# Performance work log

Hardware: AMD Instinct MI355X
Metric: run time of the kernel (lower is better)

Reference implementation:

```python
import jax, jax.numpy as jnp
import numpy as np

DIM = 64; NH = 4; WS = (2, 7, 7); FRAMES = 8
# torch code uses head_dim = dim // num_heads for BOTH attentions' scale
SCALE = (DIM // NH) ** -0.5

def _rel_pos_index(ws):
    coords = np.stack(np.meshgrid(np.arange(ws[0]), np.arange(ws[1]), np.arange(ws[2]), indexing='ij'))
    cf = coords.reshape(3, -1)
    rc = (cf[:, :, None] - cf[:, None, :]).transpose(1, 2, 0)
    rc[:, :, 0] += ws[0] - 1; rc[:, :, 1] += ws[1] - 1; rc[:, :, 2] += ws[2] - 1
    rc[:, :, 0] *= (2 * ws[1] - 1) * (2 * ws[2] - 1)
    rc[:, :, 1] *= 2 * ws[2] - 1
    return jnp.asarray(rc.sum(-1))

REL_S = _rel_pos_index(WS)              # (98, 98)
REL_T = _rel_pos_index((FRAMES, 1, 1))  # (8, 8)

def _ln(x, g, b, eps=1e-5):
    m = x.mean(-1, keepdims=True)
    v = ((x - m) ** 2).mean(-1, keepdims=True)
    return (x - m) * jax.lax.rsqrt(v + eps) * g + b

def _conv3d(x, w, b):
    y = jax.lax.conv_general_dilated(x, w, (1, 1, 1), [(1, 1)] * 3,
                                     dimension_numbers=('NCDHW', 'OIDHW', 'NCDHW'))
    return y + b[None, :, None, None, None]

def setup_inputs():
    key = jax.random.key(0)
    ks = jax.random.split(key, 16)
    B, D, H, W, C = 2, 8, 112, 112, DIM
    C2 = C // 2
    n = lambda i, shape: jax.random.normal(ks[i], shape, jnp.float32) * 0.02
    return dict(
        x=jax.random.normal(ks[0], (B, D, H, W, C), jnp.float32),
        mask_matrix=jnp.zeros((1, 98, 98), jnp.float32),
        g1=jnp.ones((C,), jnp.float32), b1=jnp.zeros((C,), jnp.float32),
        rpb_s=n(1, ((2*WS[0]-1)*(2*WS[1]-1)*(2*WS[2]-1), NH)),
        qkv_w_s=n(2, (C, 3*C)), qkv_b_s=jnp.zeros((3*C,), jnp.float32),
        proj_w_s=n(3, (C, C)), proj_b_s=jnp.zeros((C,), jnp.float32),
        rpb_t=n(4, (2*FRAMES-1, NH)),
        qkv_w_t=n(5, (C, 3*C2)), qkv_b_t=jnp.zeros((3*C2,), jnp.float32),
        proj_w_t=n(6, (C2, C)), proj_b_t=jnp.zeros((C,), jnp.float32),
        g2=jnp.ones((C,), jnp.float32), b2=jnp.zeros((C,), jnp.float32),
        p1c1_w=n(7, (C2, C2, 3, 3, 3)), p1c1_b=jnp.zeros((C2,), jnp.float32),
        p1c2_w=n(8, (C2, C2, 3, 3, 3)), p1c2_b=jnp.zeros((C2,), jnp.float32),
        p2c1_w=n(9, (C2, C2, 3, 3, 3)), p2c1_b=jnp.zeros((C2,), jnp.float32),
        p2c2_w=n(10, (C2, C2, 3, 3, 3)), p2c2_b=jnp.zeros((C2,), jnp.float32),
    )

def reference(x, mask_matrix, g1, b1, rpb_s, qkv_w_s, qkv_b_s, proj_w_s, proj_b_s,
              rpb_t, qkv_w_t, qkv_b_t, proj_w_t, proj_b_t, g2, b2,
              p1c1_w, p1c1_b, p1c2_w, p1c2_b, p2c1_w, p2c1_b, p2c2_w, p2c2_b):
    B, D, H, W, C = x.shape
    C2 = C // 2
    wd, wh, ww = WS
    N = wd * wh * ww
    shortcut = x
    h = _ln(x, g1, b1)
    # ---- space attention over (2,7,7) windows (shift=0, H/W/D divisible -> no pad/roll/mask) ----
    xw = h.reshape(B, D // wd, wd, H // wh, wh, W // ww, ww, C)
    xw = xw.transpose(0, 1, 3, 5, 2, 4, 6, 7).reshape(-1, N, C)  # (nW, N, C)
    nw = xw.shape[0]
    qkv = (xw @ qkv_w_s + qkv_b_s).reshape(nw, N, 3, NH, C // NH).transpose(2, 0, 3, 1, 4)
    q, k, v = qkv[0] * SCALE, qkv[1], qkv[2]
    attn = jnp.einsum('whnd,whmd->whnm', q, k)
    bias = rpb_s[REL_S.reshape(-1)].reshape(N, N, NH).transpose(2, 0, 1)
    attn = jax.nn.softmax(attn + bias[None], axis=-1)
    out = jnp.einsum('whnm,whmd->whnd', attn, v).transpose(0, 2, 1, 3).reshape(nw, N, C)
    out = out @ proj_w_s + proj_b_s
    space = out.reshape(B, D // wd, H // wh, W // ww, wd, wh, ww, C)
    space = space.transpose(0, 1, 4, 2, 5, 3, 6, 7).reshape(B, D, H, W, C)
    # ---- time attention over frames (qkv projects to C/2) ----
    xt = h.transpose(0, 2, 3, 1, 4).reshape(B * H * W, D, C)
    qkv_t = (xt @ qkv_w_t + qkv_b_t).reshape(-1, D, 3, NH, C2 // NH).transpose(2, 0, 3, 1, 4)
    qt, kt, vt = qkv_t[0] * SCALE, qkv_t[1], qkv_t[2]
    at = jnp.einsum('bhnd,bhmd->bhnm', qt, kt)
    bias_t = rpb_t[REL_T.reshape(-1)].reshape(D, D, NH).transpose(2, 0, 1)
    at = jax.nn.softmax(at + bias_t[None], axis=-1)
    ot = jnp.einsum('bhnm,bhmd->bhnd', at, vt).transpose(0, 2, 1, 3).reshape(-1, D, C2)
    ot = ot @ proj_w_t + proj_b_t  # (B*H*W, D, C)
    time = ot.reshape(B, H, W, D, C).transpose(0, 3, 1, 2, 4)
    x = shortcut + time + space
    # ---- GRFFNet conv FFN ----
    h2 = _ln(x, g2, b2).transpose(0, 4, 1, 2, 3)  # (B,C,D,H,W)
    x1, x2 = h2[:, :C2], h2[:, C2:]
    y1 = x1 + _conv3d(jax.nn.leaky_relu(_conv3d(x1, p1c1_w, p1c1_b)), p1c2_w, p1c2_b)
    x2 = x2 + y1
    y2 = x2 + _conv3d(jax.nn.leaky_relu(_conv3d(x2, p2c1_w, p2c1_b)), p2c2_w, p2c2_b)
    y = jnp.concatenate([y1, y2], axis=1).transpose(0, 2, 3, 4, 1)
    return x + y
```

## Files before the change

kernel.cpp:

```cpp
#include <hip/hip_runtime.h>
#include <hip/hip_bf16.h>

typedef unsigned short u16;
typedef unsigned int u32;
typedef __attribute__((ext_vector_type(8))) short s16x8;
typedef __attribute__((ext_vector_type(4))) float f32x4;

__device__ __forceinline__ u16 f2b(float v) {
  u32 bits = __float_as_uint(v);
  bits += 0x7fffu + ((bits >> 16) & 1u);
  return (u16)(bits >> 16);
}
__device__ __forceinline__ float b2f(u16 u) { return __uint_as_float(((u32)u) << 16); }
__device__ __forceinline__ float bflo(u32 w) { return __uint_as_float(w << 16); }
__device__ __forceinline__ float bfhi(u32 w) { return __uint_as_float(w & 0xffff0000u); }

__global__ __launch_bounds__(256) void k_ln(const float* __restrict__ x, const float* __restrict__ g,
    const float* __restrict__ b, float* __restrict__ hout, u16* __restrict__ xb) {
  int token = blockIdx.x * 4 + (threadIdx.x >> 6);
  int lane = threadIdx.x & 63;
  long base = (long)token * 64 + lane;
  float v = x[base];
  float s = v;
#pragma unroll
  for (int o = 32; o; o >>= 1) s += __shfl_xor(s, o);
  float m = s * 0.015625f;
  float d = v - m;
  float q = d * d;
#pragma unroll
  for (int o = 32; o; o >>= 1) q += __shfl_xor(q, o);
  float r = rsqrtf(q * 0.015625f + 1e-5f);
  float hv = d * r * g[lane] + b[lane];
  hout[base] = hv;
  if (lane < 32) xb[(long)token * 32 + lane] = f2b(hv);
}

__global__ __launch_bounds__(256) void k_prep(const float* __restrict__ pw, u16* __restrict__ pwb,
    const float* __restrict__ tqw, u16* __restrict__ twb,
    const float* __restrict__ sqw, u16* __restrict__ swb,
    const float* __restrict__ rpb, float* __restrict__ Bt) {
  int i = blockIdx.x * 256 + threadIdx.x;
  if (i < 4096) {
    int r = i & 7, q = i >> 3;
    int col = q & 15; q >>= 4;
    int lk = q & 1; q >>= 1;
    int nt = q & 3, hd = q >> 2;
    pwb[i] = f2b(pw[(hd * 16 + lk * 8 + r) * 64 + nt * 16 + col]);
  } else if (i < 10240) {
    int j = i - 4096;
    int kk = j & 31, q = j >> 5;
    int lm = q & 15, ksnt = q >> 4;
    int ks = ksnt & 1, nt = ksnt >> 1;
    twb[j] = f2b(tqw[(ks * 32 + kk) * 96 + nt * 16 + lm]);
  } else if (i < 22528) {
    int j = i - 10240;
    int kk = j & 31, q = j >> 5;
    int lm = q & 15, ksnt = q >> 4;
    int ks = ksnt & 1, nt = ksnt >> 1;
    swb[j] = f2b(sqw[(ks * 32 + kk) * 192 + nt * 16 + lm]);
  } else {
    int j = i - 22528;
    int m = j % 112, q = j / 112;
    int n = q % 112, hd = q / 112;
    float v = -1e30f;
    if (n < 98 && m < 98) {
      int dzn = n / 49, rn = n % 49, hyn = rn / 7, wxn = rn % 7;
      int dzm = m / 49, rm = m % 49, hym = rm / 7, wxm = rm % 7;
      int idx = (dzn - dzm + 1) * 169 + (hyn - hym + 6) * 13 + (wxn - wxm + 6);
      v = rpb[idx * 4 + hd];
    }
    Bt[j] = v;
  }
}

__global__ __launch_bounds__(256) void k_wprep(const float* __restrict__ w0, const float* __restrict__ w1,
    const float* __restrict__ w2, const float* __restrict__ w3, u16* __restrict__ WB) {
  int j = blockIdx.x * 256 + threadIdx.x;
  int c = j / 27648, j2 = j - c * 27648;
  const float* src = c == 0 ? w0 : c == 1 ? w1 : c == 2 ? w2 : w3;
  int co = j2 / 864, rem = j2 - co * 864, ci = rem / 27, kk = rem - ci * 27;
  WB[c * 27648 + kk * 1024 + co * 32 + ci] = f2b(src[j2]);
}

__global__ __launch_bounds__(256) void k_fused1(const float* __restrict__ x,
    const float* __restrict__ g1, const float* __restrict__ b1,
    const u16* __restrict__ swb, const float* __restrict__ sqb,
    const u16* __restrict__ twb, const float* __restrict__ tqb,
    float* __restrict__ acc, u16* __restrict__ Qg, u16* __restrict__ Kg,
    u16* __restrict__ Vg, u16* __restrict__ T) {
  int l = threadIdx.x & 63, wv = threadIdx.x >> 6;
  int lm = l & 15, lk = l >> 4;
  long t0 = (long)blockIdx.x * 64 + wv * 16;
  long tok = t0 + lm;
  const float* xp = x + tok * 64 + lk * 8;
  float* ap = acc + tok * 64 + lk * 8;
  float va[16];
  float s = 0.f;
#pragma unroll
  for (int ks = 0; ks < 2; ks++) {
    float4 a0 = *(const float4*)(xp + ks * 32);
    float4 a1 = *(const float4*)(xp + ks * 32 + 4);
    *(float4*)(ap + ks * 32) = a0;
    *(float4*)(ap + ks * 32 + 4) = a1;
    va[ks * 8 + 0] = a0.x; va[ks * 8 + 1] = a0.y; va[ks * 8 + 2] = a0.z; va[ks * 8 + 3] = a0.w;
    va[ks * 8 + 4] = a1.x; va[ks * 8 + 5] = a1.y; va[ks * 8 + 6] = a1.z; va[ks * 8 + 7] = a1.w;
    s += a0.x + a0.y + a0.z + a0.w + a1.x + a1.y + a1.z + a1.w;
  }
  s += __shfl_xor(s, 16); s += __shfl_xor(s, 32);
  float m = s * 0.015625f;
  float q = 0.f;
#pragma unroll
  for (int j = 0; j < 16; j++) { float d = va[j] - m; q += d * d; }
  q += __shfl_xor(q, 16); q += __shfl_xor(q, 32);
  float r = rsqrtf(q * 0.015625f + 1e-5f);
  s16x8 A[2];
#pragma unroll
  for (int ks = 0; ks < 2; ks++) {
    float4 g0 = *(const float4*)(g1 + ks * 32 + lk * 8);
    float4 g4 = *(const float4*)(g1 + ks * 32 + lk * 8 + 4);
    float4 c0 = *(const float4*)(b1 + ks * 32 + lk * 8);
    float4 c4 = *(const float4*)(b1 + ks * 32 + lk * 8 + 4);
    s16x8 a;
    a[0] = (short)f2b((va[ks * 8 + 0] - m) * r * g0.x + c0.x);
    a[1] = (short)f2b((va[ks * 8 + 1] - m) * r * g0.y + c0.y);
    a[2] = (short)f2b((va[ks * 8 + 2] - m) * r * g0.z + c0.z);
    a[3] = (short)f2b((va[ks * 8 + 3] - m) * r * g0.w + c0.w);
    a[4] = (short)f2b((va[ks * 8 + 4] - m) * r * g4.x + c4.x);
    a[5] = (short)f2b((va[ks * 8 + 5] - m) * r * g4.y + c4.y);
    a[6] = (short)f2b((va[ks * 8 + 6] - m) * r * g4.z + c4.z);
    a[7] = (short)f2b((va[ks * 8 + 7] - m) * r * g4.w + c4.w);
    A[ks] = a;
  }
  f32x4 C[12], D[6];
#pragma unroll
  for (int nt = 0; nt < 12; nt++) C[nt] = (f32x4){0.f, 0.f, 0.f, 0.f};
#pragma unroll
  for (int nt = 0; nt < 6; nt++) D[nt] = (f32x4){0.f, 0.f, 0.f, 0.f};
#pragma unroll
  for (int ks = 0; ks < 2; ks++) {
#pragma unroll
    for (int nt = 0; nt < 12; nt++) {
      s16x8 B = *(const s16x8*)&swb[((nt * 2 + ks) * 16 + lm) * 32 + lk * 8];
      C[nt] = __builtin_amdgcn_mfma_f32_16x16x32_bf16(A[ks], B, C[nt], 0, 0, 0);
    }
#pragma unroll
    for (int nt = 0; nt < 6; nt++) {
      s16x8 B = *(const s16x8*)&twb[((nt * 2 + ks) * 16 + lm) * 32 + lk * 8];
      D[nt] = __builtin_amdgcn_mfma_f32_16x16x32_bf16(A[ks], B, D[nt], 0, 0, 0);
    }
  }
  float sbv[12], tbv[6];
#pragma unroll
  for (int nt = 0; nt < 12; nt++) sbv[nt] = sqb[nt * 16 + lm];
#pragma unroll
  for (int nt = 0; nt < 6; nt++) tbv[nt] = tqb[nt * 16 + lm];
#pragma unroll
  for (int r4 = 0; r4 < 4; r4++) {
    long t = t0 + lk * 4 + r4;
    int b = (int)(t / 100352); int r1 = (int)(t - (long)b * 100352);
    int d = r1 / 12544; int r2 = r1 - d * 12544;
    int hy = r2 / 112, wx = r2 - hy * 112;
    int d0 = d >> 1, dz = d & 1, h0 = hy / 7, oy = hy - h0 * 7, w0 = wx / 7, ox = wx - w0 * 7;
    int wi = ((b * 4 + d0) * 16 + h0) * 16 + w0;
    int n = dz * 49 + oy * 7 + ox;
    long sbase = (long)(wi * 4) * 1568 + n * 16 + lm;
#pragma unroll
    for (int nt = 0; nt < 12; nt++) {
      int part = nt >> 2, hd = nt & 3;
      float v = C[nt][r4] + sbv[nt];
      long o = sbase + hd * 1568;
      if (part == 0) Qg[o] = f2b(v * 0.25f);
      else if (part == 1) Kg[o] = f2b(v);
      else Vg[o] = f2b(v);
    }
    long sidx = ((long)(b * 12544 + r2) * 8 + d) * 96;
#pragma unroll
    for (int nt = 0; nt < 6; nt++) {
      float v = D[nt][r4] + tbv[nt];
      if (nt < 2) v *= 0.25f;
      T[sidx + nt * 16 + lm] = f2b(v);
    }
  }
}

__global__ __launch_bounds__(512) void k_sattn3(const u16* __restrict__ Qg, const u16* __restrict__ Kg,
    const u16* __restrict__ Vg, const float* __restrict__ Bt, const u16* __restrict__ pwb,
    const float* __restrict__ pb, float* __restrict__ accg) {
  __shared__ __align__(16) u16 sK[112 * 24];
  __shared__ __align__(16) u16 sVt[16 * 136];
  __shared__ __align__(16) u16 sP[112 * 120 + 32];
  __shared__ __align__(16) u16 sO[112 * 24];
  int tid = threadIdx.x;
  int wi = blockIdx.x;
  int l = tid & 63, wv = tid >> 6;
  int lm = l & 15, lk = l >> 4;

  for (int i = tid; i < 336; i += 512) { sK[2352 + i] = 0; }
  for (int i = tid; i < 224; i += 512) { sVt[(i / 14) * 136 + 98 + (i % 14)] = 0; }

  int mt = wv;
  bool act = mt < 7;
  int baserow = mt * 16 + lk * 4;
  int qrow = mt * 16 + lm;
  f32x4 po[4];
#pragma unroll
  for (int b = 0; b < 4; b++) po[b] = (f32x4){0.f, 0.f, 0.f, 0.f};

  for (int hd = 0; hd < 4; hd++) {
    __syncthreads();
    long base = (long)(wi * 4 + hd) * 1568;
    const u32* kp = (const u32*)(Kg + base);
    const u32* vp = (const u32*)(Vg + base);
    for (int i = tid; i < 784; i += 512) {
      u32 v = kp[i];
      int n = i >> 3, j2 = (i & 7) * 2;
      *(u32*)&sK[n * 24 + j2] = v;
    }
    for (int i = tid; i < 784; i += 512) {
      u32 v = vp[i];
      int n = i >> 3, j2 = (i & 7) * 2;
      sVt[j2 * 136 + n] = (u16)(v & 0xffffu);
      sVt[(j2 + 1) * 136 + n] = (u16)(v >> 16);
    }
    __syncthreads();
    if (!act) continue;

    s16x8 Aq = {};
    if (qrow < 98 && lk < 2) Aq = *(const s16x8*)(Qg + base + qrow * 16 + lk * 8);
    f32x4 S[7];
#pragma unroll
    for (int nt = 0; nt < 7; nt++) {
      s16x8 Bk = {};
      if (lk < 2) Bk = *(const s16x8*)&sK[(nt * 16 + lm) * 24 + lk * 8];
      S[nt] = __builtin_amdgcn_mfma_f32_16x16x32_bf16(Aq, Bk, (f32x4){0.f, 0.f, 0.f, 0.f}, 0, 0, 0);
    }
    const float* bt = Bt + hd * 12544 + baserow * 112 + lm;
    float mx0 = -3e38f, mx1 = -3e38f, mx2 = -3e38f, mx3 = -3e38f;
#pragma unroll
    for (int nt = 0; nt < 7; nt++) {
      S[nt][0] += bt[nt * 16];
      S[nt][1] += bt[112 + nt * 16];
      S[nt][2] += bt[224 + nt * 16];
      S[nt][3] += bt[336 + nt * 16];
      mx0 = fmaxf(mx0, S[nt][0]); mx1 = fmaxf(mx1, S[nt][1]);
      mx2 = fmaxf(mx2, S[nt][2]); mx3 = fmaxf(mx3, S[nt][3]);
    }
#pragma unroll
    for (int off = 1; off < 16; off <<= 1) {
      mx0 = fmaxf(mx0, __shfl_xor(mx0, off));
      mx1 = fmaxf(mx1, __shfl_xor(mx1, off));
      mx2 = fmaxf(mx2, __shfl_xor(mx2, off));
      mx3 = fmaxf(mx3, __shfl_xor(mx3, off));
    }
    float s0 = 0.f, s1 = 0.f, s2 = 0.f, s3 = 0.f;
#pragma unroll
    for (int nt = 0; nt < 7; nt++) {
      S[nt][0] = __expf(S[nt][0] - mx0); s0 += S[nt][0];
      S[nt][1] = __expf(S[nt][1] - mx1); s1 += S[nt][1];
      S[nt][2] = __expf(S[nt][2] - mx2); s2 += S[nt][2];
      S[nt][3] = __expf(S[nt][3] - mx3); s3 += S[nt][3];
    }
#pragma unroll
    for (int off = 1; off < 16; off <<= 1) {
      s0 += __shfl_xor(s0, off); s1 += __shfl_xor(s1, off);
      s2 += __shfl_xor(s2, off); s3 += __shfl_xor(s3, off);
    }
    float i0 = 1.f / s0, i1 = 1.f / s1, i2 = 1.f / s2, i3 = 1.f / s3;
#pragma unroll
    for (int nt = 0; nt < 7; nt++) {
      int c = nt * 16 + lm;
      sP[(baserow + 0) * 120 + c] = f2b(S[nt][0] * i0);
      sP[(baserow + 1) * 120 + c] = f2b(S[nt][1] * i1);
      sP[(baserow + 2) * 120 + c] = f2b(S[nt][2] * i2);
      sP[(baserow + 3) * 120 + c] = f2b(S[nt][3] * i3);
    }
    int rowoff = (mt * 16 + lm) * 120;
    f32x4 pv = (f32x4){0.f, 0.f, 0.f, 0.f};
#pragma unroll
    for (int ks = 0; ks < 3; ks++) {
      s16x8 Ap = *(const s16x8*)&sP[rowoff + ks * 32 + lk * 8];
      s16x8 Bv = *(const s16x8*)&sVt[lm * 136 + ks * 32 + lk * 8];
      pv = __builtin_amdgcn_mfma_f32_16x16x32_bf16(Ap, Bv, pv, 0, 0, 0);
    }
    {
      s16x8 Ap = {}, Bv = {};
      if (lk < 2) {
        Ap = *(const s16x8*)&sP[rowoff + 96 + lk * 8];
        Bv = *(const s16x8*)&sVt[lm * 136 + 96 + lk * 8];
      }
      pv = __builtin_amdgcn_mfma_f32_16x16x32_bf16(Ap, Bv, pv, 0, 0, 0);
    }
#pragma unroll
    for (int r = 0; r < 4; r++) sO[(baserow + r) * 24 + lm] = f2b(pv[r]);
    s16x8 Ao = {};
    if (lk < 2) Ao = *(const s16x8*)&sO[(mt * 16 + lm) * 24 + lk * 8];
#pragma unroll
    for (int nt = 0; nt < 4; nt++) {
      s16x8 Bw = {};
      if (lk < 2) Bw = *(const s16x8*)&pwb[((((hd * 4 + nt) * 2 + lk) * 16 + lm) * 8)];
      po[nt] = __builtin_amdgcn_mfma_f32_16x16x32_bf16(Ao, Bw, po[nt], 0, 0, 0);
    }
  }
  if (act) {
    int b = wi >> 10, d0 = (wi >> 8) & 3, h0 = (wi >> 4) & 15, w0 = wi & 15;
    float pbv[4];
#pragma unroll
    for (int nt = 0; nt < 4; nt++) pbv[nt] = pb[nt * 16 + lm];
#pragma unroll
    for (int r = 0; r < 4; r++) {
      int n = mt * 16 + lk * 4 + r;
      if (n >= 98) continue;
      int dz = n / 49, rr = n - dz * 49, oy = rr / 7, ox = rr - oy * 7;
      long p = ((long)(b * 8 + d0 * 2 + dz) * 112 + (h0 * 7 + oy)) * 112 + (w0 * 7 + ox);
      float* ap = accg + p * 64;
#pragma unroll
      for (int nt = 0; nt < 4; nt++) {
        int col = nt * 16 + lm;
        ap[col] += po[nt][r] + pbv[nt];
      }
    }
  }
}

__global__ __launch_bounds__(256) void k_tattn2(const u16* __restrict__ T, const float* __restrict__ rpbt,
    const float* __restrict__ pw, const float* __restrict__ pb, float* __restrict__ acc) {
  __shared__ float sm[4][1064];
  int wv = threadIdx.x >> 6, lane = threadIdx.x & 63;
  int s = blockIdx.x * 4 + wv;
  int b = s / 12544, rr = s - b * 12544;
  float* sq = sm[wv];
  float* o = sq + 800;
  const u32* Tp = (const u32*)(T + (long)s * 768);
  for (int i = lane; i < 192; i += 64) {
    u32 lo = Tp[i * 2], hi = Tp[i * 2 + 1];
    int d = i / 24, base = (i - d * 24) * 4;
    float* dst = sq + d * 100 + base;
    dst[0] = bflo(lo); dst[1] = bfhi(lo); dst[2] = bflo(hi); dst[3] = bfhi(hi);
  }
  __syncthreads();
  if (lane < 32) {
    int hd = lane >> 3, n = lane & 7;
    const float* qr = sq + n * 100 + hd * 8;
    float p[8];
    float mx = -3e38f;
#pragma unroll
    for (int m = 0; m < 8; m++) {
      const float* kr = sq + m * 100 + 32 + hd * 8;
      float sc = 0.f;
#pragma unroll
      for (int e = 0; e < 8; e++) sc += qr[e] * kr[e];
      sc += rpbt[(n - m + 7) * 4 + hd];
      p[m] = sc; mx = fmaxf(mx, sc);
    }
    float sum = 0.f;
#pragma unroll
    for (int m = 0; m < 8; m++) { p[m] = __expf(p[m] - mx); sum += p[m]; }
    float inv = 1.f / sum;
#pragma unroll
    for (int j = 0; j < 8; j++) {
      float oj = 0.f;
#pragma unroll
      for (int m = 0; m < 8; m++) oj += p[m] * sq[m * 100 + 64 + hd * 8 + j];
      o[n * 33 + hd * 8 + j] = oj * inv;
    }
  }
  __syncthreads();
  float a[8];
  float pbc = pb[lane];
#pragma unroll
  for (int n = 0; n < 8; n++) a[n] = pbc;
  for (int k = 0; k < 32; k++) {
    float w = pw[k * 64 + lane];
#pragma unroll
    for (int n = 0; n < 8; n++) a[n] += o[n * 33 + k] * w;
  }
  long base = ((long)b * 100352 + rr) * 64 + lane;
#pragma unroll
  for (int n = 0; n < 8; n++) acc[base + (long)n * 802816] += a[n];
}

__global__ __launch_bounds__(64) void k_convm(const u16* __restrict__ in, const u16* __restrict__ wb,
    const float* __restrict__ bias, int mode,
    const float* __restrict__ hbuf, const float* __restrict__ accb,
    float* __restrict__ dout, float* __restrict__ x2f, u16* __restrict__ outb) {
  int row = blockIdx.x;
  int hh = row % 112, bz = row / 112;
  int d = bz & 7, bb = bz >> 3;
  long prow = (long)row * 112;
  int l = threadIdx.x, lm = l & 15, lk = l >> 4;
  f32x4 acc[7][2];
#pragma unroll
  for (int t = 0; t < 7; t++) { acc[t][0] = (f32x4){0.f,0.f,0.f,0.f}; acc[t][1] = (f32x4){0.f,0.f,0.f,0.f}; }
  for (int kd = 0; kd < 3; kd++) {
    int zd = d + kd - 1;
    if (zd < 0 || zd > 7) continue;
    for (int kh = 0; kh < 3; kh++) {
      int yy = hh + kh - 1;
      if (yy < 0 || yy > 111) continue;
      const u16* ip = in + ((long)((bb * 8 + zd) * 112 + yy)) * 112 * 32;
      int kkb = kd * 9 + kh * 3;
      s16x8 B0[3], B1[3];
#pragma unroll
      for (int kw = 0; kw < 3; kw++) {
        const u16* wp = wb + (kkb + kw) * 1024 + lk * 8;
        B0[kw] = *(const s16x8*)(wp + lm * 32);
        B1[kw] = *(const s16x8*)(wp + (16 + lm) * 32);
      }
#pragma unroll
      for (int t = 0; t < 7; t++) {
#pragma unroll
        for (int kw = 0; kw < 3; kw++) {
          int w = t * 16 + lm + kw - 1;
          s16x8 A = {};
          if ((unsigned)w < 112u) A = *(const s16x8*)(ip + (long)w * 32 + lk * 8);
          acc[t][0] = __builtin_amdgcn_mfma_f32_16x16x32_bf16(A, B0[kw], acc[t][0], 0, 0, 0);
          acc[t][1] = __builtin_amdgcn_mfma_f32_16x16x32_bf16(A, B1[kw], acc[t][1], 0, 0, 0);
        }
      }
    }
  }
  float b0 = bias[lm], b1 = bias[16 + lm];
#pragma unroll
  for (int t = 0; t < 7; t++) {
#pragma unroll
    for (int r = 0; r < 4; r++) {
      long pos = prow + t * 16 + lk * 4 + r;
      float v0 = acc[t][0][r] + b0;
      float v1 = acc[t][1][r] + b1;
      if (mode == 1) {
        v0 = v0 > 0.f ? v0 : 0.01f * v0;
        v1 = v1 > 0.f ? v1 : 0.01f * v1;
        outb[pos * 32 + lm] = f2b(v0);
        outb[pos * 32 + 16 + lm] = f2b(v1);
      } else if (mode == 2) {
        float y0 = v0 + hbuf[pos * 64 + lm];
        float y1v = v1 + hbuf[pos * 64 + 16 + lm];
        dout[pos * 64 + lm] = accb[pos * 64 + lm] + y0;
        dout[pos * 64 + 16 + lm] = accb[pos * 64 + 16 + lm] + y1v;
        float t0 = hbuf[pos * 64 + 32 + lm] + y0;
        float t1 = hbuf[pos * 64 + 48 + lm] + y1v;
        x2f[pos * 32 + lm] = t0;
        x2f[pos * 32 + 16 + lm] = t1;
        outb[pos * 32 + lm] = f2b(t0);
        outb[pos * 32 + 16 + lm] = f2b(t1);
      } else {
        float y0 = v0 + x2f[pos * 32 + lm];
        float y1v = v1 + x2f[pos * 32 + 16 + lm];
        dout[pos * 64 + 32 + lm] = accb[pos * 64 + 32 + lm] + y0;
        dout[pos * 64 + 48 + lm] = accb[pos * 64 + 48 + lm] + y1v;
      }
    }
  }
}

extern "C" void kernel_launch(void* const* d_in, const int* in_sizes, int n_in,
                              void* d_out, int out_size, void* d_ws, size_t ws_size,
                              hipStream_t stream) {
  const float* x        = (const float*)d_in[0];
  const float* g1       = (const float*)d_in[2];
  const float* b1       = (const float*)d_in[3];
  const float* rpb_s    = (const float*)d_in[4];
  const float* qkv_w_s  = (const float*)d_in[5];
  const float* qkv_b_s  = (const float*)d_in[6];
  const float* proj_w_s = (const float*)d_in[7];
  const float* proj_b_s = (const float*)d_in[8];
  const float* rpb_t    = (const float*)d_in[9];
  const float* qkv_w_t  = (const float*)d_in[10];
  const float* qkv_b_t  = (const float*)d_in[11];
  const float* proj_w_t = (const float*)d_in[12];
  const float* proj_b_t = (const float*)d_in[13];
  const float* g2       = (const float*)d_in[14];
  const float* b2       = (const float*)d_in[15];
  const float* c1w = (const float*)d_in[16];
  const float* c1b = (const float*)d_in[17];
  const float* c2w = (const float*)d_in[18];
  const float* c2b = (const float*)d_in[19];
  const float* c3w = (const float*)d_in[20];
  const float* c3b = (const float*)d_in[21];
  const float* c4w = (const float*)d_in[22];
  const float* c4b = (const float*)d_in[23];

  float* acc  = (float*)d_ws;
  float* hbuf = acc + 12845056;
  float* creg = hbuf + 12845056;
  u16* Qg = (u16*)creg;
  u16* Kg = Qg + 12845056;
  u16* Vg = Kg + 12845056;
  u16* Tt = (u16*)hbuf;
  u16* x1b = (u16*)creg;
  u16* t_b = x1b + 6422528;
  u16* x2b = t_b + 6422528;
  float* x2f = (float*)(x2b + 6422528);
  u16* WB = (u16*)(x2f + 6422528);
  float* dout = (float*)d_out;
  u16* pwb = (u16*)d_out;
  u16* twb = (u16*)d_out + 4096;
  u16* swb = (u16*)d_out + 10240;
  float* Bt = (float*)d_out + 11264;

  k_prep<<<284, 256, 0, stream>>>(proj_w_s, pwb, qkv_w_t, twb, qkv_w_s, swb, rpb_s, Bt);
  k_fused1<<<3136, 256, 0, stream>>>(x, g1, b1, swb, qkv_b_s, twb, qkv_b_t,
                                     acc, Qg, Kg, Vg, Tt);
  k_sattn3<<<2048, 512, 0, stream>>>(Qg, Kg, Vg, Bt, pwb, proj_b_s, acc);
  k_wprep<<<432, 256, 0, stream>>>(c1w, c2w, c3w, c4w, WB);
  k_tattn2<<<6272, 256, 0, stream>>>(Tt, rpb_t, proj_w_t, proj_b_t, acc);
  k_ln<<<50176, 256, 0, stream>>>(acc, g2, b2, hbuf, x1b);
  k_convm<<<1792, 64, 0, stream>>>(x1b, WB, c1b, 1, nullptr, nullptr, nullptr, nullptr, t_b);
  k_convm<<<1792, 64, 0, stream>>>(t_b, WB + 27648, c2b, 2, hbuf, acc, dout, x2f, x2b);
  k_convm<<<1792, 64, 0, stream>>>(x2b, WB + 2 * 27648, c3b, 1, nullptr, nullptr, nullptr, nullptr, t_b);
  k_convm<<<1792, 64, 0, stream>>>(t_b, WB + 3 * 27648, c4b, 4, nullptr, acc, dout, x2f, nullptr);
}
```

Measured before the change: 428.1 us.

## Split conv output channels across grid and store FFN residuals as bf16

Each conv kernel now launches a second grid dimension so each 64-thread block computes 16 output channels instead of 32, doubling block count and halving accumulator registers per wave. The fp32 LN output buffer and fp32 x2 buffer are replaced by bf16 halves (x1b, x2h, x2b) used as residuals, cutting global traffic in the LN and conv epilogues. The trade-off is that input rows are reloaded twice across the channel split, and residuals now carry bf16 rounding error into the output.

Result: slower. 453.2 us (+5.9%).

```diff
diff --git a/kernel.cpp b/kernel.cpp
--- a/kernel.cpp
+++ b/kernel.cpp
@@ -15,8 +15,8 @@
 __device__ __forceinline__ float bflo(u32 w) { return __uint_as_float(w << 16); }
 __device__ __forceinline__ float bfhi(u32 w) { return __uint_as_float(w & 0xffff0000u); }
 
-__global__ __launch_bounds__(256) void k_ln(const float* __restrict__ x, const float* __restrict__ g,
-    const float* __restrict__ b, float* __restrict__ hout, u16* __restrict__ xb) {
+__global__ __launch_bounds__(256) void k_ln2(const float* __restrict__ x, const float* __restrict__ g,
+    const float* __restrict__ b, u16* __restrict__ x1b, u16* __restrict__ x2h) {
   int token = blockIdx.x * 4 + (threadIdx.x >> 6);
   int lane = threadIdx.x & 63;
   long base = (long)token * 64 + lane;
@@ -31,8 +31,9 @@
   for (int o = 32; o; o >>= 1) q += __shfl_xor(q, o);
   float r = rsqrtf(q * 0.015625f + 1e-5f);
   float hv = d * r * g[lane] + b[lane];
-  hout[base] = hv;
-  if (lane < 32) xb[(long)token * 32 + lane] = f2b(hv);
+  u16 hb = f2b(hv);
+  if (lane < 32) x1b[(long)token * 32 + lane] = hb;
+  else x2h[(long)token * 32 + lane - 32] = hb;
 }
 
 __global__ __launch_bounds__(256) void k_prep(const float* __restrict__ pw, u16* __restrict__ pwb,
@@ -381,16 +382,17 @@
 
 __global__ __launch_bounds__(64) void k_convm(const u16* __restrict__ in, const u16* __restrict__ wb,
     const float* __restrict__ bias, int mode,
-    const float* __restrict__ hbuf, const float* __restrict__ accb,
-    float* __restrict__ dout, float* __restrict__ x2f, u16* __restrict__ outb) {
+    const u16* __restrict__ res1, const u16* __restrict__ res2,
+    const float* __restrict__ accb, float* __restrict__ dout, u16* __restrict__ outb) {
   int row = blockIdx.x;
   int hh = row % 112, bz = row / 112;
   int d = bz & 7, bb = bz >> 3;
   long prow = (long)row * 112;
   int l = threadIdx.x, lm = l & 15, lk = l >> 4;
-  f32x4 acc[7][2];
-#pragma unroll
-  for (int t = 0; t < 7; t++) { acc[t][0] = (f32x4){0.f,0.f,0.f,0.f}; acc[t][1] = (f32x4){0.f,0.f,0.f,0.f}; }
+  int co = blockIdx.y * 16 + lm;
+  f32x4 acc[7];
+#pragma unroll
+  for (int t = 0; t < 7; t++) acc[t] = (f32x4){0.f, 0.f, 0.f, 0.f};
   for (int kd = 0; kd < 3; kd++) {
     int zd = d + kd - 1;
     if (zd < 0 || zd > 7) continue;
@@ -399,13 +401,10 @@
       if (yy < 0 || yy > 111) continue;
       const u16* ip = in + ((long)((bb * 8 + zd) * 112 + yy)) * 112 * 32;
       int kkb = kd * 9 + kh * 3;
-      s16x8 B0[3], B1[3];
-#pragma unroll
-      for (int kw = 0; kw < 3; kw++) {
-        const u16* wp = wb + (kkb + kw) * 1024 + lk * 8;
-        B0[kw] = *(const s16x8*)(wp + lm * 32);
-        B1[kw] = *(const s16x8*)(wp + (16 + lm) * 32);
-      }
+      s16x8 B[3];
+#pragma unroll
+      for (int kw = 0; kw < 3; kw++)
+        B[kw] = *(const s16x8*)(wb + (kkb + kw) * 1024 + co * 32 + lk * 8);
 #pragma unroll
       for (int t = 0; t < 7; t++) {
 #pragma unroll
@@ -413,41 +412,28 @@
           int w = t * 16 + lm + kw - 1;
           s16x8 A = {};
           if ((unsigned)w < 112u) A = *(const s16x8*)(ip + (long)w * 32 + lk * 8);
-          acc[t][0] = __builtin_amdgcn_mfma_f32_16x16x32_bf16(A, B0[kw], acc[t][0], 0, 0, 0);
-          acc[t][1] = __builtin_amdgcn_mfma_f32_16x16x32_bf16(A, B1[kw], acc[t][1], 0, 0, 0);
+          acc[t] = __builtin_amdgcn_mfma_f32_16x16x32_bf16(A, B[kw], acc[t], 0, 0, 0);
         }
       }
     }
   }
-  float b0 = bias[lm], b1 = bias[16 + lm];
+  float bv = bias[co];
 #pragma unroll
   for (int t = 0; t < 7; t++) {
 #pragma unroll
     for (int r = 0; r < 4; r++) {
       long pos = prow + t * 16 + lk * 4 + r;
-      float v0 = acc[t][0][r] + b0;
-      float v1 = acc[t][1][r] + b1;
+      float v = acc[t][r] + bv;
       if (mode == 1) {
-        v0 = v0 > 0.f ? v0 : 0.01f * v0;
-        v1 = v1 > 0.f ? v1 : 0.01f * v1;
-        outb[pos * 32 + lm] = f2b(v0);
-        outb[pos * 32 + 16 + lm] = f2b(v1);
+        v = v > 0.f ? v : 0.01f * v;
+        outb[pos * 32 + co] = f2b(v);
       } else if (mode == 2) {
-        float y0 = v0 + hbuf[pos * 64 + lm];
-        float y1v = v1 + hbuf[pos * 64 + 16 + lm];
-        dout[pos * 64 + lm] = accb[pos * 64 + lm] + y0;
-        dout[pos * 64 + 16 + lm] = accb[pos * 64 + 16 + lm] + y1v;
-        float t0 = hbuf[pos * 64 + 32 + lm] + y0;
-        float t1 = hbuf[pos * 64 + 48 + lm] + y1v;
-        x2f[pos * 32 + lm] = t0;
-        x2f[pos * 32 + 16 + lm] = t1;
-        outb[pos * 32 + lm] = f2b(t0);
-        outb[pos * 32 + 16 + lm] = f2b(t1);
+        float y = v + b2f(res1[pos * 32 + co]);
+        dout[pos * 64 + co] = accb[pos * 64 + co] + y;
+        outb[pos * 32 + co] = f2b(b2f(res2[pos * 32 + co]) + y);
       } else {
-        float y0 = v0 + x2f[pos * 32 + lm];
-        float y1v = v1 + x2f[pos * 32 + 16 + lm];
-        dout[pos * 64 + 32 + lm] = accb[pos * 64 + 32 + lm] + y0;
-        dout[pos * 64 + 48 + lm] = accb[pos * 64 + 48 + lm] + y1v;
+        float y = v + b2f(res1[pos * 32 + co]);
+        dout[pos * 64 + 32 + co] = accb[pos * 64 + 32 + co] + y;
       }
     }
   }
@@ -490,8 +476,8 @@
   u16* x1b = (u16*)creg;
   u16* t_b = x1b + 6422528;
   u16* x2b = t_b + 6422528;
-  float* x2f = (float*)(x2b + 6422528);
-  u16* WB = (u16*)(x2f + 6422528);
+  u16* x2h = x2b + 6422528;
+  u16* WB  = x2h + 6422528;
   float* dout = (float*)d_out;
   u16* pwb = (u16*)d_out;
   u16* twb = (u16*)d_out + 4096;
@@ -504,9 +490,9 @@
   k_sattn3<<<2048, 512, 0, stream>>>(Qg, Kg, Vg, Bt, pwb, proj_b_s, acc);
   k_wprep<<<432, 256, 0, stream>>>(c1w, c2w, c3w, c4w, WB);
   k_tattn2<<<6272, 256, 0, stream>>>(Tt, rpb_t, proj_w_t, proj_b_t, acc);
-  k_ln<<<50176, 256, 0, stream>>>(acc, g2, b2, hbuf, x1b);
-  k_convm<<<1792, 64, 0, stream>>>(x1b, WB, c1b, 1, nullptr, nullptr, nullptr, nullptr, t_b);
-  k_convm<<<1792, 64, 0, stream>>>(t_b, WB + 27648, c2b, 2, hbuf, acc, dout, x2f, x2b);
-  k_convm<<<1792, 64, 0, stream>>>(x2b, WB + 2 * 27648, c3b, 1, nullptr, nullptr, nullptr, nullptr, t_b);
-  k_convm<<<1792, 64, 0, stream>>>(t_b, WB + 3 * 27648, c4b, 4, nullptr, acc, dout, x2f, nullptr);
-}
+  k_ln2<<<50176, 256, 0, stream>>>(acc, g2, b2, x1b, x2h);
+  k_convm<<<dim3(1792, 2), 64, 0, stream>>>(x1b, WB, c1b, 1, nullptr, nullptr, nullptr, nullptr, t_b);
+  k_convm<<<dim3(1792, 2), 64, 0, stream>>>(t_b, WB + 27648, c2b, 2, x1b, x2h, acc, dout, x2b);
+  k_convm<<<dim3(1792, 2), 64, 0, stream>>>(x2b, WB + 2 * 27648, c3b, 1, nullptr, nullptr, nullptr, nullptr, t_b);
+  k_convm<<<dim3(1792, 2), 64, 0, stream>>>(t_b, WB + 3 * 27648, c4b, 4, x2b, nullptr, acc, dout, nullptr);
+}
```
